# Kernel tuning notes

Hardware: AMD Instinct MI355X
Metric: run time of the kernel (lower is better)

## Reference

```python
import jax, jax.numpy as jnp
import numpy as np

B, S, D, H, HID = 2, 2048, 256, 8, 1024
EPS = 1e-9


def gelu_fast(x):
    return 0.5 * x * (1.0 + jnp.tanh(x * 0.7978845608 * (1.0 + 0.044715 * x * x)))


def layer_norm(x, g, b):
    m = jnp.mean(x, axis=-1, keepdims=True)
    v = jnp.mean(jnp.square(x - m), axis=-1, keepdims=True)
    return (x - m) * jax.lax.rsqrt(v + EPS) * g + b


def setup_inputs() -> dict:
    key = jax.random.key(0)
    ks = jax.random.split(key, 16)
    x = jax.random.normal(ks[0], (B, S, D), dtype=jnp.float32)
    # causal look-ahead mask: additive, 0 on/below diagonal, -1e9 above
    causal = jnp.triu(jnp.ones((S, S), dtype=jnp.float32), k=1) * (-1e9)
    look_ahead_mask = causal[None, None, :, :]  # (1,1,S,S)
    sd = 0.02
    return {
        "x": x,
        "look_ahead_mask": look_ahead_mask,
        "ln1_g": jnp.ones((D,), jnp.float32),
        "ln1_b": jnp.zeros((D,), jnp.float32),
        "wq_w": jax.random.normal(ks[1], (D * H, D), jnp.float32) * sd,
        "wq_b": jnp.zeros((D * H,), jnp.float32),
        "wk_w": jax.random.normal(ks[2], (D * H, D), jnp.float32) * sd,
        "wk_b": jnp.zeros((D * H,), jnp.float32),
        "wv_w": jax.random.normal(ks[3], (D * H, D), jnp.float32) * sd,
        "wv_b": jnp.zeros((D * H,), jnp.float32),
        "dense_w": jax.random.normal(ks[4], (D, D * H), jnp.float32) * sd,
        "dense_b": jnp.zeros((D,), jnp.float32),
        "ln2_g": jnp.ones((D,), jnp.float32),
        "ln2_b": jnp.zeros((D,), jnp.float32),
        "fc1_w": jax.random.normal(ks[5], (HID, D), jnp.float32) * sd,
        "fc1_b": jnp.zeros((HID,), jnp.float32),
        "fc2_w": jax.random.normal(ks[6], (D, HID), jnp.float32) * sd,
        "fc2_b": jnp.zeros((D,), jnp.float32),
    }


def reference(x, look_ahead_mask, ln1_g, ln1_b, wq_w, wq_b, wk_w, wk_b,
              wv_w, wv_b, dense_w, dense_b, ln2_g, ln2_b,
              fc1_w, fc1_b, fc2_w, fc2_b):
    xn = layer_norm(x, ln1_g, ln1_b)
    # QKV: D -> D*H, each head has full head-dim D (module quirk)
    q = (jnp.einsum('bsd,ed->bse', xn, wq_w) + wq_b).reshape(B, S, H, D).transpose(0, 2, 1, 3)
    k = (jnp.einsum('bsd,ed->bse', xn, wk_w) + wk_b).reshape(B, S, H, D).transpose(0, 2, 1, 3)
    v = (jnp.einsum('bsd,ed->bse', xn, wv_w) + wv_b).reshape(B, S, H, D).transpose(0, 2, 1, 3)
    scores = jnp.einsum('bhqd,bhkd->bhqk', q, k) / jnp.sqrt(jnp.float32(D))
    scores = scores + look_ahead_mask
    attn_weights = jax.nn.softmax(scores, axis=-1)
    ctx = jnp.einsum('bhqk,bhkd->bhqd', attn_weights, v)  # (B,H,S,D)
    ctx = ctx.transpose(0, 2, 1, 3).reshape(B, S, H * D)
    attn = jnp.einsum('bse,de->bsd', ctx, dense_w) + dense_b
    x1 = xn + attn  # residual uses post-LN x (module quirk)
    m = layer_norm(x1, ln2_g, ln2_b)
    m = gelu_fast(jnp.einsum('bsd,hd->bsh', m, fc1_w) + fc1_b)
    m = jnp.einsum('bsh,dh->bsd', m, fc2_w) + fc2_b
    out = x1 + m
    return out, attn_weights
```

## Files before the change

### kernel.cpp

```cpp
#include <hip/hip_runtime.h>
#include <hip/hip_bf16.h>


typedef __bf16 bf16_t;
typedef __bf16 bf16x8 __attribute__((ext_vector_type(8)));
typedef __bf16 bf16x4 __attribute__((ext_vector_type(4)));
typedef float  f32x4  __attribute__((ext_vector_type(4)));

#define DEV __device__ __forceinline__

DEV f32x4 mfma16(bf16x8 a, bf16x8 b, f32x4 c) {
  return __builtin_amdgcn_mfma_f32_16x16x32_bf16(a, b, c, 0, 0, 0);
}

DEV void gload16(const void* g, void* l) {
  __builtin_amdgcn_global_load_lds(
      (const __attribute__((address_space(1))) unsigned int*)g,
      (__attribute__((address_space(3))) unsigned int*)l, 16, 0, 0);
}

__global__ __launch_bounds__(256) void k1_lncvt(
    const float* __restrict__ x, const float* __restrict__ g, const float* __restrict__ bta,
    float* __restrict__ of, bf16_t* __restrict__ ob,
    const float* __restrict__ s0, const float* __restrict__ s1,
    const float* __restrict__ s2, const float* __restrict__ s3,
    const float* __restrict__ s4, const float* __restrict__ s5,
    bf16_t* __restrict__ d0, bf16_t* __restrict__ d1, bf16_t* __restrict__ d2,
    bf16_t* __restrict__ d3, bf16_t* __restrict__ d4, bf16_t* __restrict__ d5) {
  int bid = blockIdx.x;
  if (bid < 1024) {
    int row = bid * 4 + (threadIdx.x >> 6);
    int l = threadIdx.x & 63;
    const float4 v = *(const float4*)(x + (size_t)row * 256 + l * 4);
    float s  = v.x + v.y + v.z + v.w;
    float s2 = v.x*v.x + v.y*v.y + v.z*v.z + v.w*v.w;
#pragma unroll
    for (int o = 1; o < 64; o <<= 1) { s += __shfl_xor(s, o, 64); s2 += __shfl_xor(s2, o, 64); }
    float m   = s * (1.f/256.f);
    float var = s2 * (1.f/256.f) - m * m;
    float rs  = rsqrtf(var + 1e-9f);
    const float4 gv = *(const float4*)(g   + l * 4);
    const float4 bv = *(const float4*)(bta + l * 4);
    float4 y;
    y.x = (v.x - m) * rs * gv.x + bv.x;
    y.y = (v.y - m) * rs * gv.y + bv.y;
    y.z = (v.z - m) * rs * gv.z + bv.z;
    y.w = (v.w - m) * rs * gv.w + bv.w;
    *(float4*)(of + (size_t)row * 256 + l * 4) = y;
    bf16x4 yb = { (bf16_t)y.x, (bf16_t)y.y, (bf16_t)y.z, (bf16_t)y.w };
    *(bf16x4*)(ob + (size_t)row * 256 + l * 4) = yb;
  } else {
    int i = (bid - 1024) * 256 + threadIdx.x;
    const float* s; bf16_t* d; int off;
    if      (i < 131072) { s = s0; d = d0; off = i; }
    else if (i < 262144) { s = s1; d = d1; off = i - 131072; }
    else if (i < 393216) { s = s2; d = d2; off = i - 262144; }
    else if (i < 524288) { s = s3; d = d3; off = i - 393216; }
    else if (i < 589824) { s = s4; d = d4; off = i - 524288; }
    else                 { s = s5; d = d5; off = i - 589824; }
    float4 v = ((const float4*)s)[off];
    bf16x4 o = { (bf16_t)v.x, (bf16_t)v.y, (bf16_t)v.z, (bf16_t)v.w };
    ((bf16x4*)d)[off] = o;
  }
}

DEV void gemm_core(const bf16_t* __restrict__ A, const bf16_t* __restrict__ W,
                   int lda, int row0, int col0, int k0, int kiters,
                   char* Asb, char* Bsb, f32x4 (&acc)[4][4]) {
  int tid = threadIdx.x, w = tid >> 6, l = tid & 63, l15 = l & 15, lhi = l >> 4;
  int wr = (w >> 1) * 64, wc = (w & 1) * 64;

#define STAGE(buf, kk) do {                                                   \
    char* Ad = Asb + (buf) * 8192 + w * 1024;                                 \
    char* Bd = Bsb + (buf) * 8192 + w * 1024;                                 \
    _Pragma("unroll")                                                         \
    for (int j = 0; j < 2; ++j) {                                             \
      int idx = (j * 256 + tid) * 8; int r = idx >> 5, c = idx & 31;          \
      gload16(A + (size_t)(row0 + r) * lda + (kk) + c, Ad + j * 4096);        \
      gload16(W + (size_t)(col0 + r) * lda + (kk) + c, Bd + j * 4096);        \
    } } while (0)

  STAGE(0, k0);
  for (int t = 0; t < kiters; ++t) {
    int cur = t & 1;
    if (t + 1 < kiters) {
      STAGE(cur ^ 1, k0 + (t + 1) * 32);
      asm volatile("s_waitcnt vmcnt(4)" ::: "memory");
    } else {
      asm volatile("s_waitcnt vmcnt(0)" ::: "memory");
    }
    __builtin_amdgcn_s_barrier();
    asm volatile("" ::: "memory");
    const bf16_t* As = (const bf16_t*)(Asb + cur * 8192);
    const bf16_t* Bs = (const bf16_t*)(Bsb + cur * 8192);
    bf16x8 af[4], bfr[4];
#pragma unroll
    for (int m = 0; m < 4; ++m)
      af[m] = *(const bf16x8*)(As + (wr + 16 * m + l15) * 32 + lhi * 8);
#pragma unroll
    for (int n = 0; n < 4; ++n)
      bfr[n] = *(const bf16x8*)(Bs + (wc + 16 * n + l15) * 32 + lhi * 8);
#pragma unroll
    for (int m = 0; m < 4; ++m)
#pragma unroll
      for (int n = 0; n < 4; ++n)
        acc[m][n] = mfma16(af[m], bfr[n], acc[m][n]);
    asm volatile("s_waitcnt lgkmcnt(0)" ::: "memory");
    __builtin_amdgcn_s_barrier();
  }
#undef STAGE
}

__global__ __launch_bounds__(256, 4) void gemm_qkv(
    const bf16_t* __restrict__ A,
    const bf16_t* __restrict__ W0, const bf16_t* __restrict__ W1, const bf16_t* __restrict__ W2,
    const float* __restrict__ b0, const float* __restrict__ b1, const float* __restrict__ b2,
    bf16_t* __restrict__ qo, bf16_t* __restrict__ ko, bf16_t* __restrict__ vto) {
  __shared__ char smem[34816];
  char* Asb = smem;
  char* Bsb = smem + 16384;
  int bx = blockIdx.x;
  int wsel = bx >> 4, cb = bx & 15;
  const bf16_t* W    = wsel == 0 ? W0 : (wsel == 1 ? W1 : W2);
  const float*  bias = wsel == 0 ? b0 : (wsel == 1 ? b1 : b2);
  int row0 = blockIdx.y * 128, col0 = cb * 128;
  f32x4 acc[4][4] = {};
  gemm_core(A, W, 256, row0, col0, 0, 8, Asb, Bsb, acc);

  int tid = threadIdx.x, w = tid >> 6, l = tid & 63, l15 = l & 15, lhi = l >> 4;
  int wr = (w >> 1) * 64, wc = (w & 1) * 64;

  if (wsel < 2) {
    bf16_t* out = wsel == 0 ? qo : ko;
#pragma unroll
    for (int m = 0; m < 4; ++m)
#pragma unroll
      for (int n = 0; n < 4; ++n)
#pragma unroll
        for (int j = 0; j < 4; ++j) {
          int row = row0 + wr + 16 * m + lhi * 4 + j;
          int col = col0 + wc + 16 * n + l15;
          float v = acc[m][n][j] + bias[col];
          out[((size_t)((row >> 11) * 8 + (col >> 8)) * 2048 + (row & 2047)) * 256 + (col & 255)] = (bf16_t)v;
        }
  } else {
    __syncthreads();
    bf16_t* T = (bf16_t*)smem;
#pragma unroll
    for (int m = 0; m < 4; ++m)
#pragma unroll
      for (int n = 0; n < 4; ++n) {
        int d = wc + 16 * n + l15;
        int s = wr + 16 * m + lhi * 4;
        bf16x4 v4;
#pragma unroll
        for (int j = 0; j < 4; ++j) v4[j] = (bf16_t)(acc[m][n][j] + bias[col0 + d]);
        *(bf16x4*)(T + d * 136 + s) = v4;
      }
    __syncthreads();
    int bh = ((row0 >> 11) << 3) + (col0 >> 8);
    int d0 = col0 & 255, s0g = row0 & 2047;
#pragma unroll
    for (int p = 0; p < 8; ++p) {
      int idx = p * 256 + tid;
      int d = idx >> 4, c = (idx & 15) * 8;
      bf16x8 v8 = *(const bf16x8*)(T + d * 136 + c);
      *(bf16x8*)(vto + ((size_t)bh * 256 + d0 + d) * 2048 + s0g + c) = v8;
    }
  }
}

__global__ __launch_bounds__(256, 4) void gemm_part(
    const bf16_t* __restrict__ A, const bf16_t* __restrict__ W,
    int lda, int ksub, float* __restrict__ parts) {
  __shared__ char Asb[2 * 8192];
  __shared__ char Bsb[2 * 8192];
  int z = blockIdx.z;
  int row0 = blockIdx.y * 128, col0 = blockIdx.x * 128;
  f32x4 acc[4][4] = {};
  gemm_core(A, W, lda, row0, col0, z * ksub, ksub >> 5, Asb, Bsb, acc);

  int tid = threadIdx.x, w = tid >> 6, l = tid & 63, l15 = l & 15, lhi = l >> 4;
  int wr = (w >> 1) * 64, wc = (w & 1) * 64;
  float* p = parts + (size_t)z * 1048576;
#pragma unroll
  for (int m = 0; m < 4; ++m)
#pragma unroll
    for (int n = 0; n < 4; ++n)
#pragma unroll
      for (int j = 0; j < 4; ++j) {
        int row = row0 + wr + 16 * m + lhi * 4 + j;
        int col = col0 + wc + 16 * n + l15;
        p[(size_t)row * 256 + col] = acc[m][n][j];
      }
}

__global__ __launch_bounds__(256) void reduce4(
    const float* __restrict__ parts, const float* __restrict__ bias,
    const float* __restrict__ res, float* __restrict__ out) {
  int i = blockIdx.x * 256 + threadIdx.x;
  f32x4 s = *(const f32x4*)(parts + (size_t)i * 4);
  s += *(const f32x4*)(parts + 1048576 + (size_t)i * 4);
  s += *(const f32x4*)(parts + 2097152 + (size_t)i * 4);
  s += *(const f32x4*)(parts + 3145728 + (size_t)i * 4);
  s += *(const f32x4*)(res + (size_t)i * 4);
  s += *(const f32x4*)(bias + (i & 63) * 4);
  *(f32x4*)(out + (size_t)i * 4) = s;
}

__global__ __launch_bounds__(256) void reduce_ln(
    const float* __restrict__ parts, const float* __restrict__ bias,
    const float* __restrict__ res, const float* __restrict__ g,
    const float* __restrict__ bta, float* __restrict__ x1o, bf16_t* __restrict__ mo) {
  int row = blockIdx.x * 4 + (threadIdx.x >> 6);
  int l = threadIdx.x & 63;
  size_t base = (size_t)row * 256 + l * 4;
  f32x4 s = *(const f32x4*)(parts + base);
  s += *(const f32x4*)(parts + 1048576 + base);
  s += *(const f32x4*)(parts + 2097152 + base);
  s += *(const f32x4*)(parts + 3145728 + base);
  s += *(const f32x4*)(res + base);
  s += *(const f32x4*)(bias + l * 4);
  *(f32x4*)(x1o + base) = s;
  float sm = s[0] + s[1] + s[2] + s[3];
  float s2 = s[0]*s[0] + s[1]*s[1] + s[2]*s[2] + s[3]*s[3];
#pragma unroll
  for (int o = 1; o < 64; o <<= 1) { sm += __shfl_xor(sm, o, 64); s2 += __shfl_xor(s2, o, 64); }
  float m   = sm * (1.f/256.f);
  float var = s2 * (1.f/256.f) - m * m;
  float rs  = rsqrtf(var + 1e-9f);
  const float4 gv = *(const float4*)(g   + l * 4);
  const float4 bv = *(const float4*)(bta + l * 4);
  bf16x4 yb;
  yb[0] = (bf16_t)((s[0] - m) * rs * gv.x + bv.x);
  yb[1] = (bf16_t)((s[1] - m) * rs * gv.y + bv.y);
  yb[2] = (bf16_t)((s[2] - m) * rs * gv.z + bv.z);
  yb[3] = (bf16_t)((s[3] - m) * rs * gv.w + bv.w);
  *(bf16x4*)(mo + base) = yb;
}

__global__ __launch_bounds__(256, 4) void gemm_fc1(
    const bf16_t* __restrict__ A, const bf16_t* __restrict__ W,
    const float* __restrict__ bias, bf16_t* __restrict__ out) {
  __shared__ char Asb[2 * 8192];
  __shared__ char Bsb[2 * 8192];
  int row0 = blockIdx.y * 128, col0 = blockIdx.x * 128;
  f32x4 acc[4][4] = {};
  gemm_core(A, W, 256, row0, col0, 0, 8, Asb, Bsb, acc);

  int tid = threadIdx.x, w = tid >> 6, l = tid & 63, l15 = l & 15, lhi = l >> 4;
  int wr = (w >> 1) * 64, wc = (w & 1) * 64;
#pragma unroll
  for (int m = 0; m < 4; ++m)
#pragma unroll
    for (int n = 0; n < 4; ++n)
#pragma unroll
      for (int j = 0; j < 4; ++j) {
        int row = row0 + wr + 16 * m + lhi * 4 + j;
        int col = col0 + wc + 16 * n + l15;
        float t = acc[m][n][j] + bias[col];
        float ge = 0.5f * t * (1.f + tanhf(0.7978845608f * t * (1.f + 0.044715f * t * t)));
        out[(size_t)row * 1024 + col] = (bf16_t)ge;
      }
}

__global__ __launch_bounds__(256, 2) void attn_fused(
    const bf16_t* __restrict__ qg, const bf16_t* __restrict__ kg,
    const bf16_t* __restrict__ vt, float* __restrict__ pout,
    bf16_t* __restrict__ ctxo) {
  __shared__ __align__(16) char smem[67712];
  int bx = blockIdx.x;
  int bh = bx & 15, qt = 63 - (bx >> 4);
  int tid = threadIdx.x, w = tid >> 6, l = tid & 63;
  int l15 = l & 15, lhi = l >> 4;
  const bf16_t* Q   = qg + (size_t)bh * 2048 * 256;
  const bf16_t* Kg2 = kg + (size_t)bh * 2048 * 256;
  const bf16_t* Vt  = vt + (size_t)bh * 256 * 2048;
  int qbase = qt * 32;
  float* sl    = (float*)(smem + 65536);
  float* invsh = (float*)(smem + 67584);

  bf16x8 qf[2][8];
#pragma unroll
  for (int m = 0; m < 2; ++m)
#pragma unroll
    for (int ks = 0; ks < 8; ++ks)
      qf[m][ks] = *(const bf16x8*)(Q + (size_t)(qbase + m * 16 + l15) * 256 + ks * 32 + lhi * 8);

  char* KA = smem;
  int nktA = (qt >> 1) + 1;
#define ASTAGE(t_) do {                                                        \
    char* dst = KA + ((t_) & 1) * 32768 + w * 1024;                            \
    _Pragma("unroll")                                                          \
    for (int j = 0; j < 8; ++j) {                                              \
      int idx = (j * 256 + tid) * 16; int r = idx >> 9;                        \
      int co = (idx & 511) ^ ((r & 7) << 4);                                   \
      gload16(Kg2 + (size_t)((t_) * 64 + r) * 256 + (co >> 1), dst + j * 4096);\
    } } while (0)
  ASTAGE(0);
  if (nktA > 1) ASTAGE(1);

  float sums[2][4] = {};
  for (int t = 0; t < nktA; ++t) {
    if (t + 1 < nktA) asm volatile("s_waitcnt vmcnt(8)" ::: "memory");
    else              asm volatile("s_waitcnt vmcnt(0)" ::: "memory");
    __builtin_amdgcn_s_barrier();
    const char* Kb = KA + (t & 1) * 32768;
    int row = w * 16 + l15;
    f32x4 acc[2] = {};
    __builtin_amdgcn_s_setprio(1);
#pragma unroll
    for (int ks = 0; ks < 8; ++ks) {
      bf16x8 kb = *(const bf16x8*)(Kb + row * 512 + ((ks * 64 + lhi * 16) ^ ((row & 7) << 4)));
      acc[0] = mfma16(qf[0][ks], kb, acc[0]);
      acc[1] = mfma16(qf[1][ks], kb, acc[1]);
    }
    __builtin_amdgcn_s_setprio(0);
#pragma unroll
    for (int m = 0; m < 2; ++m)
#pragma unroll
      for (int j = 0; j < 4; ++j) {
        int qr = qbase + m * 16 + lhi * 4 + j;
        int kc = t * 64 + row;
        sums[m][j] += (kc <= qr) ? __expf(acc[m][j] * 0.0625f) : 0.f;
      }
    asm volatile("s_waitcnt lgkmcnt(0)" ::: "memory");
    __builtin_amdgcn_s_barrier();
    if (t + 2 < nktA) ASTAGE(t + 2);
  }
#undef ASTAGE

#pragma unroll
  for (int m = 0; m < 2; ++m)
#pragma unroll
    for (int j = 0; j < 4; ++j)
#pragma unroll
      for (int o = 1; o < 16; o <<= 1)
        sums[m][j] += __shfl_xor(sums[m][j], o, 64);
  if (l15 == 0)
#pragma unroll
    for (int m = 0; m < 2; ++m)
#pragma unroll
      for (int j = 0; j < 4; ++j)
        sl[w * 32 + m * 16 + lhi * 4 + j] = sums[m][j];
  __syncthreads();
  if (tid < 32)
    invsh[tid] = 1.f / (sl[tid] + sl[32 + tid] + sl[64 + tid] + sl[96 + tid]);
  __syncthreads();

  char* KB  = smem;
  char* VB  = smem + 32768;
  char* Psh = smem + 65536;
  int wm = w >> 1, wn = w & 1;
  float inv4[4];
#pragma unroll
  for (int j = 0; j < 4; ++j) inv4[j] = invsh[wm * 16 + lhi * 4 + j];

  int nktB = qt + 1;
#define BSTAGE(t_) do {                                                         \
    char* kd = KB + ((t_) & 1) * 16384 + w * 1024;                              \
    char* vd = VB + ((t_) & 1) * 16384 + w * 1024;                              \
    _Pragma("unroll")                                                           \
    for (int j = 0; j < 4; ++j) {                                               \
      int idx = (j * 256 + tid) * 16;                                           \
      { int r = idx >> 9; int co = (idx & 511) ^ ((r & 7) << 4);                \
        gload16(Kg2 + (size_t)((t_) * 32 + r) * 256 + (co >> 1), kd + j * 4096); } \
      { int r = idx >> 6; int co = (idx & 63) ^ (((r >> 2) & 3) << 4);          \
        gload16(Vt + (size_t)r * 2048 + (t_) * 32 + (co >> 1), vd + j * 4096); } \
    } } while (0)
  BSTAGE(0);
  if (nktB > 1) BSTAGE(1);

  f32x4 ctx[2][4] = {};
  for (int t = 0; t < nktB; ++t) {
    if (t + 1 >= nktB)      asm volatile("s_waitcnt vmcnt(0)" ::: "memory");
    else if (t == 0)        asm volatile("s_waitcnt vmcnt(8)" ::: "memory");
    else                    asm volatile("s_waitcnt vmcnt(9)" ::: "memory");
    __builtin_amdgcn_s_barrier();
    const char* Kb = KB + (t & 1) * 16384;
    const char* Vb = VB + (t & 1) * 16384;

    f32x4 acc = {};
    int krow = wn * 16 + l15;
    __builtin_amdgcn_s_setprio(1);
#pragma unroll
    for (int ks = 0; ks < 8; ++ks) {
      bf16x8 kb = *(const bf16x8*)(Kb + krow * 512 + ((ks * 64 + lhi * 16) ^ ((krow & 7) << 4)));
      acc = mfma16(qf[wm][ks], kb, acc);
    }
    __builtin_amdgcn_s_setprio(0);
#pragma unroll
    for (int j = 0; j < 4; ++j) {
      int rr = wm * 16 + lhi * 4 + j;
      int qr = qbase + rr;
      int kc = t * 32 + krow;
      float e = (kc <= qr) ? __expf(acc[j] * 0.0625f) * inv4[j] : 0.f;
      int addr = rr * 64 + krow * 2;
      *(bf16_t*)(Psh + (addr ^ (((rr >> 2) & 3) << 4))) = (bf16_t)e;
    }
    asm volatile("s_waitcnt lgkmcnt(0)" ::: "memory");
    __builtin_amdgcn_s_barrier();

    bf16x8 pa[2], vb[4];
#pragma unroll
    for (int m = 0; m < 2; ++m) {
      int pr = m * 16 + l15;
      pa[m] = *(const bf16x8*)(Psh + ((pr * 64 + lhi * 16) ^ (((pr >> 2) & 3) << 4)));
    }
#pragma unroll
    for (int n = 0; n < 4; ++n) {
      int vr = w * 64 + n * 16 + l15;
      vb[n] = *(const bf16x8*)(Vb + ((vr * 64 + lhi * 16) ^ (((vr >> 2) & 3) << 4)));
    }
    __builtin_amdgcn_s_setprio(1);
#pragma unroll
    for (int m = 0; m < 2; ++m)
#pragma unroll
      for (int n = 0; n < 4; ++n)
        ctx[m][n] = mfma16(pa[m], vb[n], ctx[m][n]);
    __builtin_amdgcn_s_setprio(0);

    {
      int prow = tid >> 3, chunk = tid & 7;
      const char* src = Psh + prow * 64 + ((chunk * 8) ^ (((prow >> 2) & 3) << 4));
      bf16x4 p4 = *(const bf16x4*)src;
      f32x4 o = { (float)p4[0], (float)p4[1], (float)p4[2], (float)p4[3] };
      *(f32x4*)(pout + ((size_t)bh * 2048 + qbase + prow) * 2048 + t * 32 + chunk * 4) = o;
    }
    asm volatile("s_waitcnt lgkmcnt(0)" ::: "memory");
    __builtin_amdgcn_s_barrier();
    if (t + 2 < nktB) BSTAGE(t + 2);
  }
#undef BSTAGE

  int b = bh >> 3, h = bh & 7;
#pragma unroll
  for (int m = 0; m < 2; ++m)
#pragma unroll
    for (int n = 0; n < 4; ++n)
#pragma unroll
      for (int j = 0; j < 4; ++j) {
        int qr = qbase + m * 16 + lhi * 4 + j;
        ctxo[((size_t)b * 2048 + qr) * 2048 + h * 256 + w * 64 + n * 16 + l15] = (bf16_t)ctx[m][n][j];
      }

  int zs = qbase + 32;
  for (int r = 0; r < 32; ++r) {
    size_t base2 = ((size_t)bh * 2048 + qbase + r) * 2048;
    for (int c = zs + tid * 4; c < 2048; c += 1024)
      *(float4*)(pout + base2 + c) = make_float4(0.f, 0.f, 0.f, 0.f);
  }
}

extern "C" void kernel_launch(void* const* d_in, const int* in_sizes, int n_in,
                              void* d_out, int out_size, void* d_ws, size_t ws_size,
                              hipStream_t stream) {
  const float* x     = (const float*)d_in[0];
  const float* ln1g  = (const float*)d_in[2];
  const float* ln1b  = (const float*)d_in[3];
  const float* wq_w  = (const float*)d_in[4];
  const float* wq_b  = (const float*)d_in[5];
  const float* wk_w  = (const float*)d_in[6];
  const float* wk_b  = (const float*)d_in[7];
  const float* wv_w  = (const float*)d_in[8];
  const float* wv_b  = (const float*)d_in[9];
  const float* dw    = (const float*)d_in[10];
  const float* db    = (const float*)d_in[11];
  const float* ln2g  = (const float*)d_in[12];
  const float* ln2b  = (const float*)d_in[13];
  const float* f1w   = (const float*)d_in[14];
  const float* f1b   = (const float*)d_in[15];
  const float* f2w   = (const float*)d_in[16];
  const float* f2b   = (const float*)d_in[17];

  char* ws = (char*)d_ws;
  const size_t MB = 1u << 20;
  float*  xn_f = (float*) (ws + 0 * MB);
  bf16_t* xn_b = (bf16_t*)(ws + 4 * MB);
  bf16_t* q_b  = (bf16_t*)(ws + 6 * MB);
  bf16_t* k_b  = (bf16_t*)(ws + 22 * MB);
  bf16_t* ctx_b= (bf16_t*)(ws + 38 * MB);
  bf16_t* vt_b = (bf16_t*)(ws + 54 * MB);
  float*  x1_f = (float*) (ws + 70 * MB);
  bf16_t* m_b  = (bf16_t*)(ws + 74 * MB);
  bf16_t* h_b  = (bf16_t*)(ws + 76 * MB);
  bf16_t* wq_bf = (bf16_t*)(ws + 84 * MB);
  bf16_t* wk_bf = wq_bf + 524288;
  bf16_t* wv_bf = wk_bf + 524288;
  bf16_t* dw_bf = wv_bf + 524288;
  bf16_t* f1_bf = dw_bf + 524288;
  bf16_t* f2_bf = f1_bf + 262144;
  float* parts_d = (float*)q_b;
  float* parts_f = (float*)k_b;

  float* out0 = (float*)d_out;
  float* pout = out0 + 1048576;

  k1_lncvt<<<3584, 256, 0, stream>>>(x, ln1g, ln1b, xn_f, xn_b,
                                     wq_w, wk_w, wv_w, dw, f1w, f2w,
                                     wq_bf, wk_bf, wv_bf, dw_bf, f1_bf, f2_bf);

  gemm_qkv<<<dim3(48, 32), 256, 0, stream>>>(xn_b, wq_bf, wk_bf, wv_bf,
                                             wq_b, wk_b, wv_b, q_b, k_b, vt_b);

  attn_fused<<<1024, 256, 0, stream>>>(q_b, k_b, vt_b, pout, ctx_b);

  gemm_part<<<dim3(2, 32, 4), 256, 0, stream>>>(ctx_b, dw_bf, 2048, 512, parts_d);
  reduce_ln<<<1024, 256, 0, stream>>>(parts_d, db, xn_f, ln2g, ln2b, x1_f, m_b);

  gemm_fc1<<<dim3(8, 32), 256, 0, stream>>>(m_b, f1_bf, f1b, h_b);

  gemm_part<<<dim3(2, 32, 4), 256, 0, stream>>>(h_b, f2_bf, 1024, 256, parts_f);
  reduce4<<<1024, 256, 0, stream>>>(parts_f, f2b, x1_f, out0);
}
```

Measured before the change: 236.6 us.

## Restructure causal attention kernel to 64-row query tiles with direct global K/V loads

```diff
diff --git a/kernel.cpp b/kernel.cpp
--- a/kernel.cpp
+++ b/kernel.cpp
@@ -268,68 +268,62 @@
     const bf16_t* __restrict__ qg, const bf16_t* __restrict__ kg,
     const bf16_t* __restrict__ vt, float* __restrict__ pout,
     bf16_t* __restrict__ ctxo) {
-  __shared__ __align__(16) char smem[67712];
+  __shared__ __align__(16) char smem[17408];
+  char*  Psh   = smem;
+  float* sl    = (float*)(smem + 16384);
+  float* invsh = (float*)(smem + 16896);
   int bx = blockIdx.x;
-  int bh = bx & 15, qt = 63 - (bx >> 4);
+  int bh = (bx & 7) | (((bx >> 3) & 1) << 3);
+  int qt = 31 - (bx >> 4);
   int tid = threadIdx.x, w = tid >> 6, l = tid & 63;
   int l15 = l & 15, lhi = l >> 4;
-  const bf16_t* Q   = qg + (size_t)bh * 2048 * 256;
-  const bf16_t* Kg2 = kg + (size_t)bh * 2048 * 256;
-  const bf16_t* Vt  = vt + (size_t)bh * 256 * 2048;
-  int qbase = qt * 32;
-  float* sl    = (float*)(smem + 65536);
-  float* invsh = (float*)(smem + 67584);
+  int wm = w >> 1, wn = w & 1;
+  const bf16_t* Q = qg + (size_t)bh * 2048 * 256;
+  const bf16_t* K = kg + (size_t)bh * 2048 * 256;
+  const bf16_t* V = vt + (size_t)bh * 256 * 2048;
+  int qbase = qt * 64;
 
   bf16x8 qf[2][8];
 #pragma unroll
   for (int m = 0; m < 2; ++m)
 #pragma unroll
     for (int ks = 0; ks < 8; ++ks)
-      qf[m][ks] = *(const bf16x8*)(Q + (size_t)(qbase + m * 16 + l15) * 256 + ks * 32 + lhi * 8);
-
-  char* KA = smem;
-  int nktA = (qt >> 1) + 1;
-#define ASTAGE(t_) do {                                                        \
-    char* dst = KA + ((t_) & 1) * 32768 + w * 1024;                            \
-    _Pragma("unroll")                                                          \
-    for (int j = 0; j < 8; ++j) {                                              \
-      int idx = (j * 256 + tid) * 16; int r = idx >> 9;                        \
-      int co = (idx & 511) ^ ((r & 7) << 4);                                   \
-      gload16(Kg2 + (size_t)((t_) * 64 + r) * 256 + (co >> 1), dst + j * 4096);\
-    } } while (0)
-  ASTAGE(0);
-  if (nktA > 1) ASTAGE(1);
+      qf[m][ks] = *(const bf16x8*)(Q + (size_t)(qbase + wm * 32 + m * 16 + l15) * 256 + ks * 32 + lhi * 8);
 
   float sums[2][4] = {};
-  for (int t = 0; t < nktA; ++t) {
-    if (t + 1 < nktA) asm volatile("s_waitcnt vmcnt(8)" ::: "memory");
-    else              asm volatile("s_waitcnt vmcnt(0)" ::: "memory");
-    __builtin_amdgcn_s_barrier();
-    const char* Kb = KA + (t & 1) * 32768;
-    int row = w * 16 + l15;
-    f32x4 acc[2] = {};
-    __builtin_amdgcn_s_setprio(1);
+  for (int t = 0; t <= qt; ++t) {
+    const bf16_t* Kt = K + (size_t)(t * 64 + wn * 32) * 256;
+    f32x4 acc[2][2] = {};
 #pragma unroll
     for (int ks = 0; ks < 8; ++ks) {
-      bf16x8 kb = *(const bf16x8*)(Kb + row * 512 + ((ks * 64 + lhi * 16) ^ ((row & 7) << 4)));
-      acc[0] = mfma16(qf[0][ks], kb, acc[0]);
-      acc[1] = mfma16(qf[1][ks], kb, acc[1]);
-    }
-    __builtin_amdgcn_s_setprio(0);
-#pragma unroll
-    for (int m = 0; m < 2; ++m)
-#pragma unroll
-      for (int j = 0; j < 4; ++j) {
-        int qr = qbase + m * 16 + lhi * 4 + j;
-        int kc = t * 64 + row;
-        sums[m][j] += (kc <= qr) ? __expf(acc[m][j] * 0.0625f) : 0.f;
-      }
-    asm volatile("s_waitcnt lgkmcnt(0)" ::: "memory");
-    __builtin_amdgcn_s_barrier();
-    if (t + 2 < nktA) ASTAGE(t + 2);
-  }
-#undef ASTAGE
-
+      bf16x8 kb0 = *(const bf16x8*)(Kt + (size_t)l15 * 256 + ks * 32 + lhi * 8);
+      bf16x8 kb1 = *(const bf16x8*)(Kt + (size_t)(16 + l15) * 256 + ks * 32 + lhi * 8);
+      acc[0][0] = mfma16(qf[0][ks], kb0, acc[0][0]);
+      acc[0][1] = mfma16(qf[0][ks], kb1, acc[0][1]);
+      acc[1][0] = mfma16(qf[1][ks], kb0, acc[1][0]);
+      acc[1][1] = mfma16(qf[1][ks], kb1, acc[1][1]);
+    }
+    if (t < qt) {
+#pragma unroll
+      for (int m = 0; m < 2; ++m)
+#pragma unroll
+        for (int n = 0; n < 2; ++n)
+#pragma unroll
+          for (int j = 0; j < 4; ++j)
+            sums[m][j] += __expf(acc[m][n][j] * 0.0625f);
+    } else {
+#pragma unroll
+      for (int m = 0; m < 2; ++m)
+#pragma unroll
+        for (int n = 0; n < 2; ++n)
+#pragma unroll
+          for (int j = 0; j < 4; ++j) {
+            int qr = qbase + wm * 32 + m * 16 + lhi * 4 + j;
+            int kc = t * 64 + wn * 32 + n * 16 + l15;
+            sums[m][j] += (kc <= qr) ? __expf(acc[m][n][j] * 0.0625f) : 0.f;
+          }
+    }
+  }
 #pragma unroll
   for (int m = 0; m < 2; ++m)
 #pragma unroll
@@ -342,110 +336,90 @@
     for (int m = 0; m < 2; ++m)
 #pragma unroll
       for (int j = 0; j < 4; ++j)
-        sl[w * 32 + m * 16 + lhi * 4 + j] = sums[m][j];
+        sl[wn * 64 + wm * 32 + m * 16 + lhi * 4 + j] = sums[m][j];
   __syncthreads();
-  if (tid < 32)
-    invsh[tid] = 1.f / (sl[tid] + sl[32 + tid] + sl[64 + tid] + sl[96 + tid]);
+  if (tid < 64) invsh[tid] = 1.f / (sl[tid] + sl[64 + tid]);
   __syncthreads();
 
-  char* KB  = smem;
-  char* VB  = smem + 32768;
-  char* Psh = smem + 65536;
-  int wm = w >> 1, wn = w & 1;
-  float inv4[4];
-#pragma unroll
-  for (int j = 0; j < 4; ++j) inv4[j] = invsh[wm * 16 + lhi * 4 + j];
-
-  int nktB = qt + 1;
-#define BSTAGE(t_) do {                                                         \
-    char* kd = KB + ((t_) & 1) * 16384 + w * 1024;                              \
-    char* vd = VB + ((t_) & 1) * 16384 + w * 1024;                              \
-    _Pragma("unroll")                                                           \
-    for (int j = 0; j < 4; ++j) {                                               \
-      int idx = (j * 256 + tid) * 16;                                           \
-      { int r = idx >> 9; int co = (idx & 511) ^ ((r & 7) << 4);                \
-        gload16(Kg2 + (size_t)((t_) * 32 + r) * 256 + (co >> 1), kd + j * 4096); } \
-      { int r = idx >> 6; int co = (idx & 63) ^ (((r >> 2) & 3) << 4);          \
-        gload16(Vt + (size_t)r * 2048 + (t_) * 32 + (co >> 1), vd + j * 4096); } \
-    } } while (0)
-  BSTAGE(0);
-  if (nktB > 1) BSTAGE(1);
-
-  f32x4 ctx[2][4] = {};
-  for (int t = 0; t < nktB; ++t) {
-    if (t + 1 >= nktB)      asm volatile("s_waitcnt vmcnt(0)" ::: "memory");
-    else if (t == 0)        asm volatile("s_waitcnt vmcnt(8)" ::: "memory");
-    else                    asm volatile("s_waitcnt vmcnt(9)" ::: "memory");
-    __builtin_amdgcn_s_barrier();
-    const char* Kb = KB + (t & 1) * 16384;
-    const char* Vb = VB + (t & 1) * 16384;
-
-    f32x4 acc = {};
-    int krow = wn * 16 + l15;
-    __builtin_amdgcn_s_setprio(1);
+  float inv[2][4];
+#pragma unroll
+  for (int m = 0; m < 2; ++m)
+#pragma unroll
+    for (int j = 0; j < 4; ++j)
+      inv[m][j] = invsh[wm * 32 + m * 16 + lhi * 4 + j];
+
+  f32x4 ctx[4][4] = {};
+  for (int t = 0; t <= qt; ++t) {
+    char* Pb = Psh + (t & 1) * 8192;
+    const bf16_t* Kt = K + (size_t)(t * 64 + wn * 32) * 256;
+
+    f32x4 acc[2][2] = {};
 #pragma unroll
     for (int ks = 0; ks < 8; ++ks) {
-      bf16x8 kb = *(const bf16x8*)(Kb + krow * 512 + ((ks * 64 + lhi * 16) ^ ((krow & 7) << 4)));
-      acc = mfma16(qf[wm][ks], kb, acc);
-    }
-    __builtin_amdgcn_s_setprio(0);
-#pragma unroll
-    for (int j = 0; j < 4; ++j) {
-      int rr = wm * 16 + lhi * 4 + j;
-      int qr = qbase + rr;
-      int kc = t * 32 + krow;
-      float e = (kc <= qr) ? __expf(acc[j] * 0.0625f) * inv4[j] : 0.f;
-      int addr = rr * 64 + krow * 2;
-      *(bf16_t*)(Psh + (addr ^ (((rr >> 2) & 3) << 4))) = (bf16_t)e;
-    }
+      bf16x8 kb0 = *(const bf16x8*)(Kt + (size_t)l15 * 256 + ks * 32 + lhi * 8);
+      bf16x8 kb1 = *(const bf16x8*)(Kt + (size_t)(16 + l15) * 256 + ks * 32 + lhi * 8);
+      acc[0][0] = mfma16(qf[0][ks], kb0, acc[0][0]);
+      acc[0][1] = mfma16(qf[0][ks], kb1, acc[0][1]);
+      acc[1][0] = mfma16(qf[1][ks], kb0, acc[1][0]);
+      acc[1][1] = mfma16(qf[1][ks], kb1, acc[1][1]);
+    }
+    bool full = (t < qt);
+#pragma unroll
+    for (int m = 0; m < 2; ++m)
+#pragma unroll
+      for (int n = 0; n < 2; ++n)
+#pragma unroll
+        for (int j = 0; j < 4; ++j) {
+          int rr = wm * 32 + m * 16 + lhi * 4 + j;
+          int cc = wn * 32 + n * 16 + l15;
+          float e = __expf(acc[m][n][j] * 0.0625f) * inv[m][j];
+          if (!full && cc > qbase + rr - t * 64) e = 0.f;
+          int byte = rr * 128 + cc * 2;
+          *(bf16_t*)(Pb + (byte ^ ((rr & 7) << 4))) = (bf16_t)e;
+          pout[((size_t)bh * 2048 + qbase + rr) * 2048 + t * 64 + cc] = e;
+        }
+    bf16x8 vb[4][2];
+#pragma unroll
+    for (int n4 = 0; n4 < 4; ++n4)
+#pragma unroll
+      for (int ks2 = 0; ks2 < 2; ++ks2)
+        vb[n4][ks2] = *(const bf16x8*)(V + (size_t)(w * 64 + n4 * 16 + l15) * 2048 + t * 64 + ks2 * 32 + lhi * 8);
+
     asm volatile("s_waitcnt lgkmcnt(0)" ::: "memory");
     __builtin_amdgcn_s_barrier();
-
-    bf16x8 pa[2], vb[4];
-#pragma unroll
-    for (int m = 0; m < 2; ++m) {
-      int pr = m * 16 + l15;
-      pa[m] = *(const bf16x8*)(Psh + ((pr * 64 + lhi * 16) ^ (((pr >> 2) & 3) << 4)));
-    }
-#pragma unroll
-    for (int n = 0; n < 4; ++n) {
-      int vr = w * 64 + n * 16 + l15;
-      vb[n] = *(const bf16x8*)(Vb + ((vr * 64 + lhi * 16) ^ (((vr >> 2) & 3) << 4)));
-    }
+    asm volatile("" ::: "memory");
+
     __builtin_amdgcn_s_setprio(1);
 #pragma unroll
-    for (int m = 0; m < 2; ++m)
-#pragma unroll
-      for (int n = 0; n < 4; ++n)
-        ctx[m][n] = mfma16(pa[m], vb[n], ctx[m][n]);
+    for (int ks2 = 0; ks2 < 2; ++ks2) {
+      bf16x8 pa[4];
+#pragma unroll
+      for (int m4 = 0; m4 < 4; ++m4) {
+        int pr = m4 * 16 + l15;
+        pa[m4] = *(const bf16x8*)(Pb + ((pr * 128 + ks2 * 64 + lhi * 16) ^ ((pr & 7) << 4)));
+      }
+#pragma unroll
+      for (int m4 = 0; m4 < 4; ++m4)
+#pragma unroll
+        for (int n4 = 0; n4 < 4; ++n4)
+          ctx[m4][n4] = mfma16(pa[m4], vb[n4][ks2], ctx[m4][n4]);
+    }
     __builtin_amdgcn_s_setprio(0);
-
-    {
-      int prow = tid >> 3, chunk = tid & 7;
-      const char* src = Psh + prow * 64 + ((chunk * 8) ^ (((prow >> 2) & 3) << 4));
-      bf16x4 p4 = *(const bf16x4*)src;
-      f32x4 o = { (float)p4[0], (float)p4[1], (float)p4[2], (float)p4[3] };
-      *(f32x4*)(pout + ((size_t)bh * 2048 + qbase + prow) * 2048 + t * 32 + chunk * 4) = o;
-    }
-    asm volatile("s_waitcnt lgkmcnt(0)" ::: "memory");
-    __builtin_amdgcn_s_barrier();
-    if (t + 2 < nktB) BSTAGE(t + 2);
-  }
-#undef BSTAGE
+  }
 
   int b = bh >> 3, h = bh & 7;
 #pragma unroll
-  for (int m = 0; m < 2; ++m)
-#pragma unroll
-    for (int n = 0; n < 4; ++n)
+  for (int m4 = 0; m4 < 4; ++m4)
+#pragma unroll
+    for (int n4 = 0; n4 < 4; ++n4)
 #pragma unroll
       for (int j = 0; j < 4; ++j) {
-        int qr = qbase + m * 16 + lhi * 4 + j;
-        ctxo[((size_t)b * 2048 + qr) * 2048 + h * 256 + w * 64 + n * 16 + l15] = (bf16_t)ctx[m][n][j];
+        int qr = qbase + m4 * 16 + lhi * 4 + j;
+        ctxo[((size_t)b * 2048 + qr) * 2048 + h * 256 + w * 64 + n4 * 16 + l15] = (bf16_t)ctx[m4][n4][j];
       }
 
-  int zs = qbase + 32;
-  for (int r = 0; r < 32; ++r) {
+  int zs = qbase + 64;
+  for (int r = 0; r < 64; ++r) {
     size_t base2 = ((size_t)bh * 2048 + qbase + r) * 2048;
     for (int c = zs + tid * 4; c < 2048; c += 1024)
       *(float4*)(pout + base2 + c) = make_float4(0.f, 0.f, 0.f, 0.f);
@@ -503,7 +477,7 @@
   gemm_qkv<<<dim3(48, 32), 256, 0, stream>>>(xn_b, wq_bf, wk_bf, wv_bf,
                                              wq_b, wk_b, wv_b, q_b, k_b, vt_b);
 
-  attn_fused<<<1024, 256, 0, stream>>>(q_b, k_b, vt_b, pout, ctx_b);
+  attn_fused<<<512, 256, 0, stream>>>(q_b, k_b, vt_b, pout, ctx_b);
 
   gemm_part<<<dim3(2, 32, 4), 256, 0, stream>>>(ctx_b, dw_bf, 2048, 512, parts_d);
   reduce_ln<<<1024, 256, 0, stream>>>(parts_d, db, xn_f, ln2g, ln2b, x1_f, m_b);
```

After: 317.1 us. 34.0% more time.
